# Kernel tuning notes

Measured on AMD Instinct MI355X. Metric: run time of the kernel, lower is better.

The kernel has to match this reference:

```python
import jax, jax.numpy as jnp
import numpy as np

B, N = 8, 2048
CLIP, D, BD, NC = 512, 256, 128, 10  # CLIP_EMBED_DIM, GNN_NODE_DIM, BOTTLENECK_DIM_GNN, NUM_CLASSES
LN_EPS = 1e-5


def _layer_norm(x, g, b):
    mu = jnp.mean(x, axis=-1, keepdims=True)
    var = jnp.mean(jnp.square(x - mu), axis=-1, keepdims=True)
    return (x - mu) / jnp.sqrt(var + LN_EPS) * g + b


def setup_inputs() -> dict:
    key = jax.random.key(0)
    ks = jax.random.split(key, 16)
    def w(k, shape, fan_in):
        lim = 1.0 / np.sqrt(fan_in)
        return jax.random.uniform(k, shape, jnp.float32, -lim, lim)
    return {
        "local_feat": jax.random.normal(ks[0], (B, N, CLIP), jnp.float32),
        "coords": jax.random.uniform(ks[1], (B, N, 2), jnp.float32),
        "mask": jax.random.randint(ks[2], (B, N), 0, 2).astype(bool),
        # node_encoder: Linear(CLIP->D) + LayerNorm(D)
        "enc_w": w(ks[3], (CLIP, D), CLIP), "enc_b": jnp.zeros((D,), jnp.float32),
        "enc_g": jnp.ones((D,), jnp.float32), "enc_beta": jnp.zeros((D,), jnp.float32),
        "gamma": jnp.asarray(5.0, jnp.float32),  # spatial_gamma
        "wq": w(ks[4], (D, D), D), "bq": jnp.zeros((D,), jnp.float32),
        "wk": w(ks[5], (D, D), D), "bk": jnp.zeros((D,), jnp.float32),
        "wv": w(ks[6], (D, D), D), "bv": jnp.zeros((D,), jnp.float32),
        # bottleneck: Linear(D->BD) + LayerNorm(BD)
        "bn_w": w(ks[7], (D, BD), D), "bn_b": jnp.zeros((BD,), jnp.float32),
        "bn_g": jnp.ones((BD,), jnp.float32), "bn_beta": jnp.zeros((BD,), jnp.float32),
        # classifier: Linear(BD->BD//2) + ReLU + Linear(BD//2->NC)
        "c1_w": w(ks[8], (BD, BD // 2), BD), "c1_b": jnp.zeros((BD // 2,), jnp.float32),
        "c2_w": w(ks[9], (BD // 2, NC), BD // 2), "c2_b": jnp.zeros((NC,), jnp.float32),
    }


def reference(local_feat, coords, mask, enc_w, enc_b, enc_g, enc_beta, gamma,
              wq, bq, wk, bk, wv, bv, bn_w, bn_b, bn_g, bn_beta,
              c1_w, c1_b, c2_w, c2_b):
    # node encoder: Linear + LN + ReLU -> h [B,N,D]
    h = jax.nn.relu(_layer_norm(local_feat @ enc_w + enc_b, enc_g, enc_beta))
    # pairwise euclidean distances on 2D coords (torch.cdist, under no_grad)
    xy = coords[:, :, :2]
    sq = jnp.sum(xy * xy, axis=-1)                                   # [B,N]
    d2 = sq[:, :, None] + sq[:, None, :] - 2.0 * jnp.einsum('bnd,bmd->bnm', xy, xy)
    dist = jax.lax.stop_gradient(jnp.sqrt(jnp.maximum(d2, 0.0)))     # [B,N,N]
    spatial_adj = jnp.exp(-dist * jnp.abs(gamma))
    q, k, v = h @ wq + bq, h @ wk + bk, h @ wv + bv
    scores = jnp.einsum('bnd,bmd->bnm', q, k) / jnp.sqrt(jnp.float32(D))
    attn = jax.nn.softmax(scores, axis=-1) * spatial_adj             # gated attention
    attn = jnp.where(mask[:, None, :], 0.0, attn)                    # zero masked keys
    agg = jnp.einsum('bnm,bmd->bnd', attn, v)                        # [B,N,D]
    out = jax.nn.relu(_layer_norm(agg @ bn_w + bn_b, bn_g, bn_beta)) # [B,N,BD]
    mask_v = (~mask)[:, :, None].astype(out.dtype)                   # [B,N,1]
    pooled = (out * mask_v).sum(axis=1) / jnp.maximum(mask_v.sum(axis=1), 1e-9)
    logits = jax.nn.relu(pooled @ c1_w + c1_b) @ c2_w + c2_b
    return logits, pooled
```

## Files before the change

### kernel.cpp

```cpp
#include <hip/hip_runtime.h>
#include <hip/hip_bf16.h>

typedef unsigned short ushort_t;
typedef __attribute__((ext_vector_type(8))) short s8;
typedef __attribute__((ext_vector_type(4))) float f4;

__device__ __forceinline__ unsigned short f2bf(float f) {
  union { float f; unsigned int u; } c; c.f = f;
  unsigned int r = (c.u + 0x7fffu + ((c.u >> 16) & 1u)) >> 16;
  return (unsigned short)r;
}
__device__ __forceinline__ float bf2f(ushort_t u) {
  union { unsigned int i; float f; } c; c.i = ((unsigned int)u) << 16; return c.f;
}
__device__ __forceinline__ uint4 pack8(float4 a, float4 b) {
  uint4 r;
  r.x = (unsigned)f2bf(a.x) | ((unsigned)f2bf(a.y) << 16);
  r.y = (unsigned)f2bf(a.z) | ((unsigned)f2bf(a.w) << 16);
  r.z = (unsigned)f2bf(b.x) | ((unsigned)f2bf(b.y) << 16);
  r.w = (unsigned)f2bf(b.z) | ((unsigned)f2bf(b.w) << 16);
  return r;
}
__device__ __forceinline__ float fsqrt_fast(float x) {
  float r; asm("v_sqrt_f32 %0, %1" : "=v"(r) : "v"(x)); return r;
}
__device__ __forceinline__ float fexp2_fast(float x) {
  float r; asm("v_exp_f32 %0, %1" : "=v"(r) : "v"(x)); return r;
}
__device__ __forceinline__ void dma16(const ushort_t* g, const short* l) {
  __builtin_amdgcn_global_load_lds(
      (const __attribute__((address_space(1))) unsigned int*)g,
      (__attribute__((address_space(3))) unsigned int*)(unsigned long)l,
      16, 0, 0);
}

#define LOG2E 1.44269504f

__global__ __launch_bounds__(256) void k_wt_all(
    const float* __restrict__ enc_w, const float* __restrict__ wq,
    const float* __restrict__ wk, const float* __restrict__ wv,
    const float* __restrict__ bn_w,
    ushort_t* __restrict__ enc_wT, ushort_t* __restrict__ wqkvT,
    ushort_t* __restrict__ bn_wT) {
  const int y = blockIdx.y;
  const int i = blockIdx.x * 256 + threadIdx.x;
  if (y == 0) {
    if (i < 131072) { const int n = i >> 9, k = i & 511; enc_wT[i] = f2bf(enc_w[k * 256 + n]); }
  } else if (y <= 3) {
    if (i < 65536) {
      const int n = i >> 8, k = i & 255;
      const float* src = (y == 1) ? wq : (y == 2) ? wk : wv;
      wqkvT[(y - 1) * 65536 + i] = f2bf(src[k * 256 + n]);
    }
  } else {
    if (i < 32768) { const int n = i >> 8, k = i & 255; bn_wT[i] = f2bf(bn_w[k * 128 + n]); }
  }
}

__global__ __launch_bounds__(256, 3) void k_gemm_enc(
    const float* __restrict__ A, const ushort_t* __restrict__ WT,
    const float* __restrict__ bia, const float* __restrict__ g,
    const float* __restrict__ beta, ushort_t* __restrict__ out) {
  __shared__ short Al[32 * 72];
  __shared__ short Bl[256 * 72];
  __shared__ float red1[32][2], red2[32][2];
  const int t = threadIdx.x;
  const int wv = t >> 6, lane = t & 63, l16 = lane & 15, quad = lane >> 4;
  const int wm = wv >> 1, wn = wv & 1;
  const int row0 = blockIdx.x * 32;

  f4 acc[8];
#pragma unroll
  for (int nf = 0; nf < 8; ++nf) acc[nf] = (f4){0.f, 0.f, 0.f, 0.f};

  for (int k0 = 0; k0 < 512; k0 += 64) {
    __syncthreads();
    {
      const int r = t >> 3, c8 = t & 7;
      const float* src = &A[(size_t)(row0 + r) * 512 + k0 + c8 * 8];
      *(uint4*)&Al[r * 72 + c8 * 8] =
          pack8(*(const float4*)src, *(const float4*)(src + 4));
    }
#pragma unroll
    for (int i = 0; i < 8; ++i) {
      const int ch = t + i * 256;
      const int r = ch >> 3, c8 = ch & 7;
      *(uint4*)&Bl[r * 72 + c8 * 8] =
          *(const uint4*)&WT[(size_t)r * 512 + k0 + c8 * 8];
    }
    __syncthreads();
#pragma unroll
    for (int kc = 0; kc < 2; ++kc) {
      const s8 af = *(const s8*)&Al[(wm * 16 + l16) * 72 + kc * 32 + quad * 8];
#pragma unroll
      for (int nf = 0; nf < 8; ++nf) {
        const s8 bf = *(const s8*)&Bl[(wn * 128 + nf * 16 + l16) * 72 + kc * 32 + quad * 8];
        acc[nf] = __builtin_amdgcn_mfma_f32_16x16x32_bf16(af, bf, acc[nf], 0, 0, 0);
      }
    }
  }
  float bi[8], gg[8], bb[8];
#pragma unroll
  for (int nf = 0; nf < 8; ++nf) {
    const int col = wn * 128 + nf * 16 + l16;
    bi[nf] = bia[col]; gg[nf] = g[col]; bb[nf] = beta[col];
  }
  float s1[4] = {0.f, 0.f, 0.f, 0.f}, s2[4] = {0.f, 0.f, 0.f, 0.f};
#pragma unroll
  for (int nf = 0; nf < 8; ++nf)
#pragma unroll
    for (int r = 0; r < 4; ++r) {
      const float v = acc[nf][r] + bi[nf];
      acc[nf][r] = v;
      s1[r] += v; s2[r] += v * v;
    }
#pragma unroll
  for (int m = 1; m < 16; m <<= 1) {
#pragma unroll
    for (int r = 0; r < 4; ++r) {
      s1[r] += __shfl_xor(s1[r], m);
      s2[r] += __shfl_xor(s2[r], m);
    }
  }
  if (l16 == 0) {
#pragma unroll
    for (int r = 0; r < 4; ++r) {
      const int rl = wm * 16 + quad * 4 + r;
      red1[rl][wn] = s1[r]; red2[rl][wn] = s2[r];
    }
  }
  __syncthreads();
#pragma unroll
  for (int r = 0; r < 4; ++r) {
    const int rl = wm * 16 + quad * 4 + r;
    const float mu = (red1[rl][0] + red1[rl][1]) * (1.f / 256.f);
    const float var = (red2[rl][0] + red2[rl][1]) * (1.f / 256.f) - mu * mu;
    const float rstd = rsqrtf(var + 1e-5f);
#pragma unroll
    for (int nf = 0; nf < 8; ++nf) {
      const int col = wn * 128 + nf * 16 + l16;
      const float v = (acc[nf][r] - mu) * rstd * gg[nf] + bb[nf];
      out[(size_t)(row0 + rl) * 256 + col] = f2bf(fmaxf(v, 0.f));
    }
  }
}

__global__ __launch_bounds__(256, 4) void k_gemm_qkv(
    const ushort_t* __restrict__ A, const ushort_t* __restrict__ WT,
    const float* __restrict__ bq, const float* __restrict__ bk,
    const float* __restrict__ bv,
    ushort_t* __restrict__ q, ushort_t* __restrict__ k, ushort_t* __restrict__ vt) {
  __shared__ short Al[64 * 72];
  __shared__ short Bl[128 * 72];
  const int t = threadIdx.x;
  const int wv = t >> 6, lane = t & 63, l16 = lane & 15, quad = lane >> 4;
  const int wm = wv >> 1, wn = wv & 1;
  const int row0 = blockIdx.x * 64;
  const int nb = blockIdx.y;
  const int type = nb >> 1;
  const ushort_t* wtb = WT + (size_t)nb * 128 * 256;

  f4 acc[2][4];
#pragma unroll
  for (int mf = 0; mf < 2; ++mf)
#pragma unroll
    for (int nf = 0; nf < 4; ++nf) acc[mf][nf] = (f4){0.f, 0.f, 0.f, 0.f};

  for (int k0 = 0; k0 < 256; k0 += 64) {
    __syncthreads();
#pragma unroll
    for (int i = 0; i < 2; ++i) {
      const int ch = t + i * 256;
      const int r = ch >> 3, c8 = ch & 7;
      *(uint4*)&Al[r * 72 + c8 * 8] =
          *(const uint4*)&A[(size_t)(row0 + r) * 256 + k0 + c8 * 8];
    }
#pragma unroll
    for (int i = 0; i < 4; ++i) {
      const int ch = t + i * 256;
      const int r = ch >> 3, c8 = ch & 7;
      *(uint4*)&Bl[r * 72 + c8 * 8] =
          *(const uint4*)&wtb[(size_t)r * 256 + k0 + c8 * 8];
    }
    __syncthreads();
#pragma unroll
    for (int kc = 0; kc < 2; ++kc) {
      s8 af[2];
      af[0] = *(const s8*)&Al[(wm * 32 + l16) * 72 + kc * 32 + quad * 8];
      af[1] = *(const s8*)&Al[(wm * 32 + 16 + l16) * 72 + kc * 32 + quad * 8];
#pragma unroll
      for (int nf = 0; nf < 4; ++nf) {
        const s8 bf = *(const s8*)&Bl[(wn * 64 + nf * 16 + l16) * 72 + kc * 32 + quad * 8];
        acc[0][nf] = __builtin_amdgcn_mfma_f32_16x16x32_bf16(af[0], bf, acc[0][nf], 0, 0, 0);
        acc[1][nf] = __builtin_amdgcn_mfma_f32_16x16x32_bf16(af[1], bf, acc[1][nf], 0, 0, 0);
      }
    }
  }
  const float* bias = (type == 0) ? bq : (type == 1) ? bk : bv;
#pragma unroll
  for (int nf = 0; nf < 4; ++nf) {
    const int colg = nb * 128 + wn * 64 + nf * 16 + l16;
    const int col = colg - type * 256;
    const float bi = bias[col];
    if (type == 2) {
      const int b = row0 >> 11;
#pragma unroll
      for (int mf = 0; mf < 2; ++mf) {
        const int n = (row0 & 2047) + wm * 32 + quad * 8 + mf * 4;
        ushort4 pk;
        pk.x = f2bf(acc[mf][nf][0] + bi);
        pk.y = f2bf(acc[mf][nf][1] + bi);
        pk.z = f2bf(acc[mf][nf][2] + bi);
        pk.w = f2bf(acc[mf][nf][3] + bi);
        *(ushort4*)&vt[((size_t)b * 256 + col) * 2048 + n] = pk;
      }
    } else {
      ushort_t* dst = (type == 0) ? q : k;
      const float sc = (type == 0) ? (0.0625f * LOG2E) : 1.f;
#pragma unroll
      for (int mf = 0; mf < 2; ++mf)
#pragma unroll
        for (int r = 0; r < 4; ++r) {
          const int row = row0 + wm * 32 + mf * 16 + quad * 4 + r;
          dst[(size_t)row * 256 + col] = f2bf((acc[mf][nf][r] + bi) * sc);
        }
    }
  }
}

__global__ __launch_bounds__(512, 2) void k_attn(
    const ushort_t* __restrict__ qb, const ushort_t* __restrict__ kb,
    const ushort_t* __restrict__ vtb,
    const float* __restrict__ coords, const int* __restrict__ mask,
    const float* __restrict__ gam,
    ushort_t* __restrict__ Opb, float* __restrict__ lws) {
  __shared__ short kld[2][8192];
  __shared__ short vld[2][8192];
  __shared__ __align__(16) float2 cls[512];
  __shared__ __align__(16) float  mls[512];
  const int t = threadIdx.x;
  const int wv = t >> 6, lane = t & 63, l16 = lane & 15, quad = lane >> 4;
  const int b = blockIdx.z, ks = blockIdx.y;
  const int qw = blockIdx.x * 256 + wv * 32;
  const int kbase = ks * 512;

  const ushort_t* kbb = kb + ((size_t)b * 2048 + kbase) * 256;
  const ushort_t* vbb = vtb + (size_t)b * 256 * 2048 + kbase;

  {
    const int key = t & 31, dg = t >> 5;
    dma16(kbb + (size_t)key * 256 + dg * 8, &kld[0][t * 8]);
    dma16(kbb + (size_t)key * 256 + dg * 8 + 128, &kld[0][(t + 512) * 8]);
    const int d = t & 255, kg = t >> 8;
    dma16(vbb + (size_t)d * 2048 + kg * 8, &vld[0][t * 8]);
    dma16(vbb + (size_t)d * 2048 + kg * 8 + 16, &vld[0][(t + 512) * 8]);
  }
  cls[t] = ((const float2*)coords)[b * 2048 + kbase + t];
  mls[t] = mask[b * 2048 + kbase + t] ? 0.f : 1.f;

  s8 qa[2][8];
  {
    const ushort_t* qrow = qb + ((size_t)b * 2048 + qw + l16) * 256 + quad * 8;
#pragma unroll
    for (int c = 0; c < 8; ++c) {
      qa[0][c] = *(const s8*)(qrow + c * 32);
      qa[1][c] = *(const s8*)(qrow + 16 * 256 + c * 32);
    }
  }
  float rcx[2], rcy[2];
  {
    const float2 c0 = ((const float2*)coords)[b * 2048 + qw + l16];
    const float2 c1 = ((const float2*)coords)[b * 2048 + qw + 16 + l16];
    rcx[0] = c0.x; rcy[0] = c0.y; rcx[1] = c1.x; rcy[1] = c1.y;
  }
  const float gl2 = fabsf(gam[0]) * LOG2E;

  f4 o[2][16];
#pragma unroll
  for (int h = 0; h < 2; ++h)
#pragma unroll
    for (int dt = 0; dt < 16; ++dt) o[h][dt] = (f4){0.f, 0.f, 0.f, 0.f};
  float lrun[2] = {0.f, 0.f};

  __syncthreads();

  for (int kt = 0; kt < 16; ++kt) {
    const int cur = kt & 1;

    if (kt < 15) {
      const ushort_t* kn = kbb + (size_t)(kt + 1) * 8192;
      const ushort_t* vn = vbb + (kt + 1) * 32;
      const int nb2 = cur ^ 1;
      const int key = t & 31, dg = t >> 5;
      dma16(kn + (size_t)key * 256 + dg * 8, &kld[nb2][t * 8]);
      dma16(kn + (size_t)key * 256 + dg * 8 + 128, &kld[nb2][(t + 512) * 8]);
      const int d = t & 255, kg = t >> 8;
      dma16(vn + (size_t)d * 2048 + kg * 8, &vld[nb2][t * 8]);
      dma16(vn + (size_t)d * 2048 + kg * 8 + 16, &vld[nb2][(t + 512) * 8]);
    }

    f4 sc[2][2];
    sc[0][0] = (f4){0.f, 0.f, 0.f, 0.f}; sc[0][1] = (f4){0.f, 0.f, 0.f, 0.f};
    sc[1][0] = (f4){0.f, 0.f, 0.f, 0.f}; sc[1][1] = (f4){0.f, 0.f, 0.f, 0.f};
#pragma unroll
    for (int c = 0; c < 8; ++c) {
      const s8 kf0 = *(const s8*)&kld[cur][((c * 4 + quad) * 32 + l16) * 8];
      sc[0][0] = __builtin_amdgcn_mfma_f32_16x16x32_bf16(kf0, qa[0][c], sc[0][0], 0, 0, 0);
      sc[1][0] = __builtin_amdgcn_mfma_f32_16x16x32_bf16(kf0, qa[1][c], sc[1][0], 0, 0, 0);
      const s8 kf1 = *(const s8*)&kld[cur][((c * 4 + quad) * 32 + 16 + l16) * 8];
      sc[0][1] = __builtin_amdgcn_mfma_f32_16x16x32_bf16(kf1, qa[0][c], sc[0][1], 0, 0, 0);
      sc[1][1] = __builtin_amdgcn_mfma_f32_16x16x32_bf16(kf1, qa[1][c], sc[1][1], 0, 0, 0);
    }

    s8 paf[2];
#pragma unroll
    for (int h = 0; h < 2; ++h) {
      unsigned pu[4];
#pragma unroll
      for (int s = 0; s < 2; ++s) {
        const int k0 = kt * 32 + s * 16 + quad * 4;
        const float4 c01 = *(const float4*)&cls[k0];
        const float4 c23 = *(const float4*)&cls[k0 + 2];
        const float4 mm = *(const float4*)&mls[k0];
        const float kx[4] = {c01.x, c01.z, c23.x, c23.z};
        const float ky[4] = {c01.y, c01.w, c23.y, c23.w};
        const float mv[4] = {mm.x, mm.y, mm.z, mm.w};
        float w[4];
#pragma unroll
        for (int r = 0; r < 4; ++r) {
          const float p = fexp2_fast(sc[h][s][r]);
          lrun[h] += p;
          const float dx = rcx[h] - kx[r], dy = rcy[h] - ky[r];
          const float dist = fsqrt_fast(dx * dx + dy * dy);
          w[r] = p * fexp2_fast(-gl2 * dist) * mv[r];
        }
        pu[s * 2 + 0] = (unsigned)f2bf(w[0]) | ((unsigned)f2bf(w[1]) << 16);
        pu[s * 2 + 1] = (unsigned)f2bf(w[2]) | ((unsigned)f2bf(w[3]) << 16);
      }
      union { s8 v; unsigned u[4]; } cv;
      cv.u[0] = pu[0]; cv.u[1] = pu[1]; cv.u[2] = pu[2]; cv.u[3] = pu[3];
      paf[h] = cv.v;
    }

#pragma unroll
    for (int dt = 0; dt < 16; ++dt) {
      const s8 bvf = *(const s8*)&vld[cur][(quad * 256 + dt * 16 + l16) * 8];
      o[0][dt] = __builtin_amdgcn_mfma_f32_16x16x32_bf16(paf[0], bvf, o[0][dt], 0, 0, 0);
      o[1][dt] = __builtin_amdgcn_mfma_f32_16x16x32_bf16(paf[1], bvf, o[1][dt], 0, 0, 0);
    }
    __syncthreads();
  }

  ushort_t* OpK = Opb + (size_t)ks * 4194304;
#pragma unroll
  for (int h = 0; h < 2; ++h)
#pragma unroll
    for (int dt = 0; dt < 16; ++dt)
#pragma unroll
      for (int r = 0; r < 4; ++r)
        OpK[((size_t)b * 2048 + qw + h * 16 + quad * 4 + r) * 256 + dt * 16 + l16] =
            f2bf(o[h][dt][r]);

#pragma unroll
  for (int h = 0; h < 2; ++h) {
    lrun[h] += __shfl_xor(lrun[h], 16);
    lrun[h] += __shfl_xor(lrun[h], 32);
  }
  if (quad == 0) {
    lws[ks * 16384 + b * 2048 + qw + l16] = lrun[0];
    lws[ks * 16384 + b * 2048 + qw + 16 + l16] = lrun[1];
  }
}

__global__ __launch_bounds__(256, 3) void k_gemm_bn(
    const ushort_t* __restrict__ Opb, const float* __restrict__ lws,
    const ushort_t* __restrict__ WT,
    const float* __restrict__ bia, const float* __restrict__ g,
    const float* __restrict__ beta, float* __restrict__ pooledAcc) {
  __shared__ short Al[32 * 72];
  __shared__ short Bl[128 * 72];
  __shared__ float red1[32][2], red2[32][2];
  __shared__ float sCm[32];
  const int t = threadIdx.x;
  const int wv = t >> 6, lane = t & 63, l16 = lane & 15, quad = lane >> 4;
  const int wm = wv >> 1, wn = wv & 1;
  const int row0 = blockIdx.x * 32;
  const int b = row0 >> 11;

  if (t < 32) {
    const int row = row0 + t;
    sCm[t] = 1.f / (lws[row] + lws[16384 + row] + lws[32768 + row] + lws[49152 + row]);
  }

  f4 acc[4];
#pragma unroll
  for (int nf = 0; nf < 4; ++nf) acc[nf] = (f4){0.f, 0.f, 0.f, 0.f};

  for (int k0 = 0; k0 < 256; k0 += 64) {
    __syncthreads();
    {
      const int r = t >> 3, c8 = t & 7;
      const float c0 = sCm[r];
      const size_t off = (size_t)(row0 + r) * 256 + k0 + c8 * 8;
      float e[8];
#pragma unroll
      for (int j = 0; j < 8; ++j) e[j] = 0.f;
#pragma unroll
      for (int pp = 0; pp < 4; ++pp) {
        const uint4 u = *(const uint4*)&Opb[(size_t)pp * 4194304 + off];
        e[0] += bf2f((ushort_t)(u.x & 0xffff)); e[1] += bf2f((ushort_t)(u.x >> 16));
        e[2] += bf2f((ushort_t)(u.y & 0xffff)); e[3] += bf2f((ushort_t)(u.y >> 16));
        e[4] += bf2f((ushort_t)(u.z & 0xffff)); e[5] += bf2f((ushort_t)(u.z >> 16));
        e[6] += bf2f((ushort_t)(u.w & 0xffff)); e[7] += bf2f((ushort_t)(u.w >> 16));
      }
      float4 ea = {c0 * e[0], c0 * e[1], c0 * e[2], c0 * e[3]};
      float4 eb = {c0 * e[4], c0 * e[5], c0 * e[6], c0 * e[7]};
      *(uint4*)&Al[r * 72 + c8 * 8] = pack8(ea, eb);
    }
#pragma unroll
    for (int i = 0; i < 4; ++i) {
      const int ch = t + i * 256;
      const int r = ch >> 3, c8 = ch & 7;
      *(uint4*)&Bl[r * 72 + c8 * 8] =
          *(const uint4*)&WT[(size_t)r * 256 + k0 + c8 * 8];
    }
    __syncthreads();
#pragma unroll
    for (int kc = 0; kc < 2; ++kc) {
      const s8 af = *(const s8*)&Al[(wm * 16 + l16) * 72 + kc * 32 + quad * 8];
#pragma unroll
      for (int nf = 0; nf < 4; ++nf) {
        const s8 bf = *(const s8*)&Bl[(wn * 64 + nf * 16 + l16) * 72 + kc * 32 + quad * 8];
        acc[nf] = __builtin_amdgcn_mfma_f32_16x16x32_bf16(af, bf, acc[nf], 0, 0, 0);
      }
    }
  }
  float bi[4], gg[4], bb[4];
#pragma unroll
  for (int nf = 0; nf < 4; ++nf) {
    const int col = wn * 64 + nf * 16 + l16;
    bi[nf] = bia[col]; gg[nf] = g[col]; bb[nf] = beta[col];
  }
  float s1[4] = {0.f, 0.f, 0.f, 0.f}, s2[4] = {0.f, 0.f, 0.f, 0.f};
#pragma unroll
  for (int nf = 0; nf < 4; ++nf)
#pragma unroll
    for (int r = 0; r < 4; ++r) {
      const float v = acc[nf][r] + bi[nf];
      acc[nf][r] = v;
      s1[r] += v; s2[r] += v * v;
    }
#pragma unroll
  for (int m = 1; m < 16; m <<= 1) {
#pragma unroll
    for (int r = 0; r < 4; ++r) {
      s1[r] += __shfl_xor(s1[r], m);
      s2[r] += __shfl_xor(s2[r], m);
    }
  }
  if (l16 == 0) {
#pragma unroll
    for (int r = 0; r < 4; ++r) {
      const int rl = wm * 16 + quad * 4 + r;
      red1[rl][wn] = s1[r]; red2[rl][wn] = s2[r];
    }
  }
  __syncthreads();
#pragma unroll
  for (int r = 0; r < 4; ++r) {
    const int rl = wm * 16 + quad * 4 + r;
    const float mu = (red1[rl][0] + red1[rl][1]) * (1.f / 128.f);
    const float var = (red2[rl][0] + red2[rl][1]) * (1.f / 128.f) - mu * mu;
    const float rstd = rsqrtf(var + 1e-5f);
#pragma unroll
    for (int nf = 0; nf < 4; ++nf) {
      const float v = (acc[nf][r] - mu) * rstd * gg[nf] + bb[nf];
      acc[nf][r] = fmaxf(v, 0.f);
    }
  }
  {
    float mw[4];
#pragma unroll
    for (int r = 0; r < 4; ++r) {
      const int rl = wm * 16 + quad * 4 + r;
      mw[r] = pooledAcc[1024 + row0 + rl];
    }
#pragma unroll
    for (int nf = 0; nf < 4; ++nf) {
      float s = acc[nf][0] * mw[0] + acc[nf][1] * mw[1] +
                acc[nf][2] * mw[2] + acc[nf][3] * mw[3];
      s += __shfl_xor(s, 16);
      s += __shfl_xor(s, 32);
      if (quad == 0) {
        const int col = wn * 64 + nf * 16 + l16;
        atomicAdd(&pooledAcc[b * 128 + col], s);
      }
    }
  }
}

__global__ __launch_bounds__(256) void k_maskf(const int* __restrict__ mask,
                                               float* __restrict__ pooledAcc) {
  const int i = blockIdx.x * 256 + threadIdx.x;
  if (i < 16384) pooledAcc[1024 + i] = mask[i] ? 0.f : 1.f;
  if (i < 1024) pooledAcc[i] = 0.f;
}

__global__ __launch_bounds__(128) void k_pool2_head(
    const float* __restrict__ pooledAcc, const int* __restrict__ mask,
    const float* __restrict__ c1w, const float* __restrict__ c1b,
    const float* __restrict__ c2w, const float* __restrict__ c2b,
    float* __restrict__ dout) {
  __shared__ float ps[128];
  __shared__ float h1[64];
  __shared__ float scnt[128];
  const int b = blockIdx.x, t = threadIdx.x;
  float c = 0.f;
  const int* mb = mask + b * 2048 + t * 16;
#pragma unroll
  for (int j = 0; j < 16; ++j) c += mb[j] ? 0.f : 1.f;
  scnt[t] = c;
  __syncthreads();
  for (int o2 = 64; o2 > 0; o2 >>= 1) {
    if (t < o2) scnt[t] += scnt[t + o2];
    __syncthreads();
  }
  const float cnt = scnt[0];
  const float p = pooledAcc[b * 128 + t] / fmaxf(cnt, 1e-9f);
  ps[t] = p;
  dout[80 + b * 128 + t] = p;
  __syncthreads();
  if (t < 64) {
    float acc = c1b[t];
    for (int d = 0; d < 128; ++d) acc += ps[d] * c1w[d * 64 + t];
    h1[t] = fmaxf(acc, 0.f);
  }
  __syncthreads();
  if (t < 10) {
    float a2 = c2b[t];
    for (int j = 0; j < 64; ++j) a2 += h1[j] * c2w[j * 10 + t];
    dout[b * 10 + t] = a2;
  }
}

extern "C" void kernel_launch(void* const* d_in, const int* in_sizes, int n_in,
                              void* d_out, int out_size, void* d_ws, size_t ws_size,
                              hipStream_t stream) {
  const float* lf     = (const float*)d_in[0];
  const float* coords = (const float*)d_in[1];
  const int*   mask   = (const int*)d_in[2];
  const float* enc_w  = (const float*)d_in[3];
  const float* enc_b  = (const float*)d_in[4];
  const float* enc_g  = (const float*)d_in[5];
  const float* enc_be = (const float*)d_in[6];
  const float* gamma  = (const float*)d_in[7];
  const float* wq     = (const float*)d_in[8];
  const float* bq     = (const float*)d_in[9];
  const float* wk     = (const float*)d_in[10];
  const float* bk     = (const float*)d_in[11];
  const float* wv     = (const float*)d_in[12];
  const float* bv     = (const float*)d_in[13];
  const float* bn_w   = (const float*)d_in[14];
  const float* bn_b   = (const float*)d_in[15];
  const float* bn_g   = (const float*)d_in[16];
  const float* bn_be  = (const float*)d_in[17];
  const float* c1w    = (const float*)d_in[18];
  const float* c1b    = (const float*)d_in[19];
  const float* c2w    = (const float*)d_in[20];
  const float* c2b    = (const float*)d_in[21];

  float* ws = (float*)d_ws;
  ushort_t* h_bf   = (ushort_t*)ws;
  ushort_t* q_bf   = (ushort_t*)(ws + 2097152);
  ushort_t* k_bf   = (ushort_t*)(ws + 4194304);
  ushort_t* vt_bf  = (ushort_t*)(ws + 6291456);
  ushort_t* Opb    = (ushort_t*)(ws + 8388608);
  ushort_t* enc_wT = (ushort_t*)(ws + 17825792);
  ushort_t* wqkvT  = (ushort_t*)(ws + 17891328);
  ushort_t* bn_wT  = (ushort_t*)(ws + 17989632);
  float*    lws    = ws + 18006016;
  float*    pooledAcc = ws + 18071552;
  float* out = (float*)d_out;

  k_wt_all<<<dim3(512, 5), 256, 0, stream>>>(enc_w, wq, wk, wv, bn_w,
                                             enc_wT, wqkvT, bn_wT);
  k_maskf<<<64, 256, 0, stream>>>(mask, pooledAcc);
  k_gemm_enc<<<512, 256, 0, stream>>>(lf, enc_wT, enc_b, enc_g, enc_be, h_bf);
  k_gemm_qkv<<<dim3(256, 6), 256, 0, stream>>>(h_bf, wqkvT, bq, bk, bv, q_bf, k_bf, vt_bf);
  k_attn<<<dim3(8, 4, 8), 512, 0, stream>>>(q_bf, k_bf, vt_bf, coords, mask, gamma,
                                            Opb, lws);
  k_gemm_bn<<<512, 256, 0, stream>>>(Opb, lws, bn_wT, bn_b, bn_g, bn_be, pooledAcc);
  k_pool2_head<<<8, 128, 0, stream>>>(pooledAcc, mask, c1w, c1b, c2w, c2b, out);
}
```

Before: 225.5 us.

## Triple-buffer K/V tiles in attention kernel with one barrier per tile

Moves the attention kernel's K and V tile staging from double to triple buffering in shared memory. Loads now run two tiles ahead, and the per-tile full __syncthreads is replaced by a partial `s_waitcnt vmcnt(4)` plus a raw `s_barrier`. The goal is to hide global-to-LDS latency and remove a barrier from each iteration. The cost is LDS use rising to roughly 100 KB per block. That probably no longer allows the two blocks per CU that the launch bounds request, so occupancy may drop.

```diff
diff --git a/kernel.cpp b/kernel.cpp
--- a/kernel.cpp
+++ b/kernel.cpp
@@ -234,8 +234,8 @@
     const float* __restrict__ coords, const int* __restrict__ mask,
     const float* __restrict__ gam,
     ushort_t* __restrict__ Opb, float* __restrict__ lws) {
-  __shared__ short kld[2][8192];
-  __shared__ short vld[2][8192];
+  __shared__ short kld[3][8192];
+  __shared__ short vld[3][8192];
   __shared__ __align__(16) float2 cls[512];
   __shared__ __align__(16) float  mls[512];
   const int t = threadIdx.x;
@@ -247,14 +247,19 @@
   const ushort_t* kbb = kb + ((size_t)b * 2048 + kbase) * 256;
   const ushort_t* vbb = vtb + (size_t)b * 256 * 2048 + kbase;
 
-  {
+  auto stage = [&](int tt, int ib) {
+    const ushort_t* kn = kbb + (size_t)tt * 8192;
+    const ushort_t* vn = vbb + tt * 32;
     const int key = t & 31, dg = t >> 5;
-    dma16(kbb + (size_t)key * 256 + dg * 8, &kld[0][t * 8]);
-    dma16(kbb + (size_t)key * 256 + dg * 8 + 128, &kld[0][(t + 512) * 8]);
+    dma16(kn + (size_t)key * 256 + dg * 8, &kld[ib][t * 8]);
+    dma16(kn + (size_t)key * 256 + dg * 8 + 128, &kld[ib][(t + 512) * 8]);
     const int d = t & 255, kg = t >> 8;
-    dma16(vbb + (size_t)d * 2048 + kg * 8, &vld[0][t * 8]);
-    dma16(vbb + (size_t)d * 2048 + kg * 8 + 16, &vld[0][(t + 512) * 8]);
-  }
+    dma16(vn + (size_t)d * 2048 + kg * 8, &vld[ib][t * 8]);
+    dma16(vn + (size_t)d * 2048 + kg * 8 + 16, &vld[ib][(t + 512) * 8]);
+  };
+
+  stage(0, 0);
+  stage(1, 1);
   cls[t] = ((const float2*)coords)[b * 2048 + kbase + t];
   mls[t] = mask[b * 2048 + kbase + t] ? 0.f : 1.f;
 
@@ -282,36 +287,19 @@
     for (int dt = 0; dt < 16; ++dt) o[h][dt] = (f4){0.f, 0.f, 0.f, 0.f};
   float lrun[2] = {0.f, 0.f};
 
-  __syncthreads();
-
-  for (int kt = 0; kt < 16; ++kt) {
-    const int cur = kt & 1;
-
-    if (kt < 15) {
-      const ushort_t* kn = kbb + (size_t)(kt + 1) * 8192;
-      const ushort_t* vn = vbb + (kt + 1) * 32;
-      const int nb2 = cur ^ 1;
-      const int key = t & 31, dg = t >> 5;
-      dma16(kn + (size_t)key * 256 + dg * 8, &kld[nb2][t * 8]);
-      dma16(kn + (size_t)key * 256 + dg * 8 + 128, &kld[nb2][(t + 512) * 8]);
-      const int d = t & 255, kg = t >> 8;
-      dma16(vn + (size_t)d * 2048 + kg * 8, &vld[nb2][t * 8]);
-      dma16(vn + (size_t)d * 2048 + kg * 8 + 16, &vld[nb2][(t + 512) * 8]);
-    }
-
+  auto compute_tile = [&](int kt, const short* kldc, const short* vldc) {
     f4 sc[2][2];
     sc[0][0] = (f4){0.f, 0.f, 0.f, 0.f}; sc[0][1] = (f4){0.f, 0.f, 0.f, 0.f};
     sc[1][0] = (f4){0.f, 0.f, 0.f, 0.f}; sc[1][1] = (f4){0.f, 0.f, 0.f, 0.f};
 #pragma unroll
     for (int c = 0; c < 8; ++c) {
-      const s8 kf0 = *(const s8*)&kld[cur][((c * 4 + quad) * 32 + l16) * 8];
+      const s8 kf0 = *(const s8*)&kldc[((c * 4 + quad) * 32 + l16) * 8];
       sc[0][0] = __builtin_amdgcn_mfma_f32_16x16x32_bf16(kf0, qa[0][c], sc[0][0], 0, 0, 0);
       sc[1][0] = __builtin_amdgcn_mfma_f32_16x16x32_bf16(kf0, qa[1][c], sc[1][0], 0, 0, 0);
-      const s8 kf1 = *(const s8*)&kld[cur][((c * 4 + quad) * 32 + 16 + l16) * 8];
+      const s8 kf1 = *(const s8*)&kldc[((c * 4 + quad) * 32 + 16 + l16) * 8];
       sc[0][1] = __builtin_amdgcn_mfma_f32_16x16x32_bf16(kf1, qa[0][c], sc[0][1], 0, 0, 0);
       sc[1][1] = __builtin_amdgcn_mfma_f32_16x16x32_bf16(kf1, qa[1][c], sc[1][1], 0, 0, 0);
     }
-
     s8 paf[2];
 #pragma unroll
     for (int h = 0; h < 2; ++h) {
@@ -341,15 +329,32 @@
       cv.u[0] = pu[0]; cv.u[1] = pu[1]; cv.u[2] = pu[2]; cv.u[3] = pu[3];
       paf[h] = cv.v;
     }
-
 #pragma unroll
     for (int dt = 0; dt < 16; ++dt) {
-      const s8 bvf = *(const s8*)&vld[cur][(quad * 256 + dt * 16 + l16) * 8];
+      const s8 bvf = *(const s8*)&vldc[(quad * 256 + dt * 16 + l16) * 8];
       o[0][dt] = __builtin_amdgcn_mfma_f32_16x16x32_bf16(paf[0], bvf, o[0][dt], 0, 0, 0);
       o[1][dt] = __builtin_amdgcn_mfma_f32_16x16x32_bf16(paf[1], bvf, o[1][dt], 0, 0, 0);
     }
-    __syncthreads();
-  }
+  };
+
+  __syncthreads();
+  stage(2, 2);
+  compute_tile(0, kld[0], vld[0]);
+
+  int cur = 1;
+  for (int kt = 1; kt < 15; ++kt) {
+    asm volatile("s_waitcnt vmcnt(4)" ::: "memory");
+    __builtin_amdgcn_s_barrier();
+    __builtin_amdgcn_sched_barrier(0);
+    const int nb3 = (cur + 2 >= 3) ? cur - 1 : cur + 2;
+    stage(kt + 2, nb3);
+    compute_tile(kt, kld[cur], vld[cur]);
+    cur = (cur + 1 >= 3) ? 0 : cur + 1;
+  }
+  asm volatile("s_waitcnt vmcnt(0)" ::: "memory");
+  __builtin_amdgcn_s_barrier();
+  __builtin_amdgcn_sched_barrier(0);
+  compute_tile(15, kld[cur], vld[cur]);
 
   ushort_t* OpK = Opb + (size_t)ks * 4194304;
 #pragma unroll
```

After: 219.1 us. 2.8% less time.
